# Kernel tuning notes

Hardware: AMD Instinct MI355X
Metric: run time of the kernel (lower is better)

The kernel has to match this reference:

```python
import jax, jax.numpy as jnp
import numpy as np

N_USERS = 17449
N_ITEMS = 48676
N = N_USERS + N_ITEMS  # 66125 nodes
H = 2    # heads
C = 64   # out_channels per head
D_IN = 64
E = 2_000_000
NEG_SLOPE = 0.2


def setup_inputs() -> dict:
    key = jax.random.key(0)
    ks = jax.random.split(key, 7)
    edge_index = jax.random.randint(ks[0], (2, E), 0, N, dtype=jnp.int32)
    # xavier-normal-ish init for embeddings and GAT params
    users_feature = jax.random.normal(ks[1], (N_USERS, D_IN), dtype=jnp.float32) * 0.1
    items_feature = jax.random.normal(ks[2], (N_ITEMS, D_IN), dtype=jnp.float32) * 0.1
    W = jax.random.normal(ks[3], (D_IN, H * C), dtype=jnp.float32) * (1.0 / np.sqrt(D_IN))
    att_src = jax.random.normal(ks[4], (H, C), dtype=jnp.float32) * 0.1
    att_dst = jax.random.normal(ks[5], (H, C), dtype=jnp.float32) * 0.1
    bias = jnp.zeros((H * C,), dtype=jnp.float32)
    return {
        "edge_index": edge_index,
        "users_feature": users_feature,
        "items_feature": items_feature,
        "W": W,
        "att_src": att_src,
        "att_dst": att_dst,
        "bias": bias,
    }


def reference(edge_index, users_feature, items_feature, W, att_src, att_dst, bias):
    # node features: [N, D_IN]
    x = jnp.concatenate([users_feature, items_feature], axis=0)
    # linear transform -> per-head features [N, H, C]
    h = (x @ W).reshape(N, H, C)
    # per-node attention logits [N, H]
    a_src = jnp.einsum("nhc,hc->nh", h, att_src)
    a_dst = jnp.einsum("nhc,hc->nh", h, att_dst)
    # add self loops (PyG GATConv default)
    loops = jnp.arange(N, dtype=edge_index.dtype)
    src = jnp.concatenate([edge_index[0], loops])
    dst = jnp.concatenate([edge_index[1], loops])
    # per-edge attention score [E+N, H]
    e = jax.nn.leaky_relu(a_src[src] + a_dst[dst], negative_slope=NEG_SLOPE)
    # segment softmax over destination node
    m = jax.lax.stop_gradient(jax.ops.segment_max(e, dst, num_segments=N))
    ex = jnp.exp(e - m[dst])
    denom = jax.ops.segment_sum(ex, dst, num_segments=N)
    alpha = ex / (denom[dst] + 1e-16)
    # scatter-add weighted source features -> [N, H, C]
    out = jax.ops.segment_sum(alpha[:, :, None] * h[src], dst, num_segments=N)
    # concat heads + bias -> [N, H*C]
    return out.reshape(N, H * C) + bias
```

## Files before the change

kernel.cpp:

```cpp
#include <hip/hip_runtime.h>
#include <hip/hip_fp16.h>
#include <math.h>

#define NEG_SLOPE 0.2f
#define BSHIFT 6
#define BNODES 64
#define MAXB 1056
#define CAP 2816
#define BIN_E 4096
#define SG_THREADS 256
#define RPT (CAP / SG_THREADS)

typedef unsigned short ushort8_v __attribute__((ext_vector_type(8)));
typedef short  short8_v  __attribute__((ext_vector_type(8)));
typedef float  float4_v  __attribute__((ext_vector_type(4)));

__device__ __forceinline__ unsigned short f2bf(float f) {
    unsigned u = __float_as_uint(f);
    u = (u + 0x7FFFu + ((u >> 16) & 1u)) >> 16;
    return (unsigned short)u;
}
__device__ __forceinline__ float bf2f(unsigned short b) {
    return __uint_as_float(((unsigned)b) << 16);
}
__device__ __forceinline__ float lrelu(float x) {
    return x > 0.f ? x : NEG_SLOPE * x;
}
__device__ __forceinline__ unsigned f2h_bits(float f) {
    __half_raw hr = __half_raw(__float2half_rn(f));
    return (unsigned)hr.x;
}
__device__ __forceinline__ float h2f_bits(unsigned short u) {
    __half_raw hr; hr.x = u;
    return __half2float(__half(hr));
}

__global__ __launch_bounds__(512) void k_xform_bin(
        const float* __restrict__ users,
        const float* __restrict__ items,
        const float* __restrict__ W,
        const float* __restrict__ att_src,
        const float* __restrict__ att_dst,
        unsigned short* __restrict__ hb,
        float* __restrict__ a_src,
        float* __restrict__ a_dst,
        const int* __restrict__ src,
        const int* __restrict__ dst,
        int* __restrict__ tails,
        int* __restrict__ stage_g,
        int nedges, int nbuckets, int n_users, int N,
        int nxf, int ntotal)
{
    __shared__ __align__(16) char smem[3 * MAXB * 4 + BIN_E * 4 + BIN_E * 2];

    const int tid  = threadIdx.x;
    const int lane = tid & 63;
    const int wid  = tid >> 6;

    const int bid = blockIdx.x;
    const long long num = (long long)nxf;
    const int xf_before = (int)(((long long)bid * num) / ntotal);
    const bool is_xf = ((((long long)(bid + 1) * num) / ntotal) > xf_before);

    if (!is_xf) {
        const int bin_id = bid - xf_before;
        int* cnt     = (int*)smem;
        int* runoff  = cnt + MAXB;
        int* cursor  = runoff + MAXB;
        int* stage   = cursor + MAXB;
        unsigned short* sb = (unsigned short*)(stage + BIN_E);

        const int base = bin_id * BIN_E;
        const int nvalid = min(BIN_E, nedges - base);

        for (int i = tid; i < nbuckets; i += 512) cnt[i] = 0;
        __syncthreads();

        int myrec[BIN_E / 512];
        int myb[BIN_E / 512];
        #pragma unroll
        for (int k = 0; k < BIN_E / 512; ++k) {
            int i = base + k * 512 + tid;
            if (i < nedges) {
                const int d = dst[i];
                myrec[k] = src[i] | ((d & (BNODES - 1)) << 17);
                myb[k] = d >> BSHIFT;
                atomicAdd(&cnt[myb[k]], 1);
            } else {
                myb[k] = -1;
            }
        }
        __syncthreads();

        if (wid == 0) {
            int running = 0;
            for (int b2 = 0; b2 < nbuckets; b2 += 64) {
                int idx = b2 + lane;
                int v = (idx < nbuckets) ? cnt[idx] : 0;
                int incl = v;
                #pragma unroll
                for (int off = 1; off < 64; off <<= 1) {
                    int t = __shfl_up(incl, off);
                    if (lane >= off) incl += t;
                }
                if (idx < nbuckets) runoff[idx] = running + incl - v;
                running += __shfl(incl, 63);
            }
        }
        __syncthreads();

        for (int i = tid; i < nbuckets; i += 512) cursor[i] = runoff[i];
        __syncthreads();

        #pragma unroll
        for (int k = 0; k < BIN_E / 512; ++k) {
            if (myb[k] >= 0) {
                int pos = atomicAdd(&cursor[myb[k]], 1);
                stage[pos] = myrec[k];
                sb[pos] = (unsigned short)myb[k];
            }
        }

        for (int i = tid; i < nbuckets; i += 512)
            if (cnt[i] > 0) {
                const int rb = atomicAdd(&tails[i], cnt[i]);
                runoff[i] = rb - runoff[i];
            }
        __syncthreads();

        for (int i = tid; i < nvalid; i += 512) {
            const int b = sb[i];
            const int idx = runoff[b] + i;
            if (idx < CAP)
                stage_g[(size_t)b * CAP + idx] = stage[i];
        }
        return;
    }

    unsigned short (*tile)[130] = (unsigned short (*)[130])smem;
    const int blk  = xf_before;
    const int quad = lane >> 4;
    const int l16  = lane & 15;
    const int tb   = blk * 128 + wid * 16;

    short8_v bfrag[8][2];
    #pragma unroll
    for (int t = 0; t < 8; ++t)
        #pragma unroll
        for (int h2 = 0; h2 < 2; ++h2)
            #pragma unroll
            for (int j = 0; j < 8; ++j)
                bfrag[t][h2][j] = (short)f2bf(
                    W[(h2 * 32 + quad * 8 + j) * 128 + t * 16 + l16]);

    float atts[8], attd[8];
    #pragma unroll
    for (int t = 0; t < 8; ++t) {
        atts[t] = att_src[t * 16 + l16];
        attd[t] = att_dst[t * 16 + l16];
    }

    const int arow = tb + l16;
    short8_v a0 = (short8_v)0, a1 = (short8_v)0;
    if (arow < N) {
        const float* xr = (arow < n_users)
            ? (users + (size_t)arow * 64)
            : (items + (size_t)(arow - n_users) * 64);
        const float4_v x0 = *reinterpret_cast<const float4_v*>(xr + quad * 8);
        const float4_v x1 = *reinterpret_cast<const float4_v*>(xr + quad * 8 + 4);
        const float4_v x2 = *reinterpret_cast<const float4_v*>(xr + 32 + quad * 8);
        const float4_v x3 = *reinterpret_cast<const float4_v*>(xr + 32 + quad * 8 + 4);
        #pragma unroll
        for (int j = 0; j < 4; ++j) {
            a0[j]     = (short)f2bf(x0[j]);
            a0[j + 4] = (short)f2bf(x1[j]);
            a1[j]     = (short)f2bf(x2[j]);
            a1[j + 4] = (short)f2bf(x3[j]);
        }
    }

    float4_v acc[8];
    #pragma unroll
    for (int t = 0; t < 8; ++t) {
        acc[t] = (float4_v)0.f;
        acc[t] = __builtin_amdgcn_mfma_f32_16x16x32_bf16(a0, bfrag[t][0], acc[t], 0, 0, 0);
        acc[t] = __builtin_amdgcn_mfma_f32_16x16x32_bf16(a1, bfrag[t][1], acc[t], 0, 0, 0);
    }

    const int wrow0 = tb + quad * 4;
    float s0[4] = {0,0,0,0}, s1[4] = {0,0,0,0};
    float d0[4] = {0,0,0,0}, d1[4] = {0,0,0,0};
    #pragma unroll
    for (int t = 0; t < 8; ++t) {
        #pragma unroll
        for (int r = 0; r < 4; ++r) {
            const float v = acc[t][r];
            if (t < 4) { s0[r] = fmaf(v, atts[t], s0[r]);
                         d0[r] = fmaf(v, attd[t], d0[r]); }
            else       { s1[r] = fmaf(v, atts[t], s1[r]);
                         d1[r] = fmaf(v, attd[t], d1[r]); }
            tile[wid * 16 + quad * 4 + r][t * 16 + l16] = f2bf(v);
        }
    }

    #pragma unroll
    for (int off = 1; off < 16; off <<= 1) {
        #pragma unroll
        for (int r = 0; r < 4; ++r) {
            s0[r] += __shfl_xor(s0[r], off);
            s1[r] += __shfl_xor(s1[r], off);
            d0[r] += __shfl_xor(d0[r], off);
            d1[r] += __shfl_xor(d1[r], off);
        }
    }
    if (l16 == 0) {
        #pragma unroll
        for (int r = 0; r < 4; ++r) {
            const int row = wrow0 + r;
            if (row < N) {
                a_src[row * 2]     = s0[r];
                a_src[row * 2 + 1] = s1[r];
                a_dst[row * 2]     = d0[r];
                a_dst[row * 2 + 1] = d1[r];
            }
        }
    }

    __syncthreads();
    const int base_node = blk * 128;
    const int nrem = min(128, N - base_node);
    for (int k = tid; k < nrem * 16; k += 512) {
        const int n = k >> 4, g = k & 15;
        ushort8_v v;
        #pragma unroll
        for (int j = 0; j < 8; ++j) v[j] = tile[n][g * 8 + j];
        *reinterpret_cast<ushort8_v*>(
            hb + (size_t)(base_node + n) * 128 + g * 8) = v;
    }
}

__global__ __launch_bounds__(SG_THREADS) void k_sort_gather(
        const int* __restrict__ stage_g,
        const int* __restrict__ tails,
        const float* __restrict__ a_src,
        const float* __restrict__ a_dst,
        const unsigned short* __restrict__ hb,
        const float* __restrict__ bias,
        float* __restrict__ out,
        int N)
{
    __shared__ int cnt[BNODES];
    __shared__ int off[BNODES];
    __shared__ int cursor[BNODES];
    __shared__ float adst[BNODES][2];
    __shared__ int2 lsorted[CAP];

    const int b    = blockIdx.x;
    const int tid  = threadIdx.x;
    const int lane = tid & 63;
    const int wid  = tid >> 6;
    const int node0  = b << BSHIFT;
    const int nnodes = min(BNODES, N - node0);
    const int nrec = min(tails[b], CAP);
    const int* bucket = stage_g + (size_t)b * CAP;

    if (tid < BNODES) {
        cnt[tid] = 0;
        if (tid < nnodes) {
            const float2 ad = *reinterpret_cast<const float2*>(
                a_dst + 2 * (node0 + tid));
            adst[tid][0] = ad.x;
            adst[tid][1] = ad.y;
        } else {
            adst[tid][0] = adst[tid][1] = 0.f;
        }
    }
    __syncthreads();

    int myrec[RPT];
    #pragma unroll
    for (int k = 0; k < RPT; ++k) {
        const int i = k * SG_THREADS + tid;
        if (i < nrec) {
            const int r = bucket[i];
            myrec[k] = r;
            atomicAdd(&cnt[(r >> 17) & (BNODES - 1)], 1);
        } else {
            myrec[k] = -1;
        }
    }
    __syncthreads();

    if (wid == 0) {
        const int v = cnt[lane];
        int incl = v;
        #pragma unroll
        for (int o = 1; o < 64; o <<= 1) {
            int t = __shfl_up(incl, o);
            if (lane >= o) incl += t;
        }
        off[lane] = incl - v;
        cursor[lane] = incl - v;
    }
    __syncthreads();

    #pragma unroll
    for (int k = 0; k < RPT; ++k) {
        const int r = myrec[k];
        if (r >= 0) {
            const int s = r & 0x1FFFF;
            const int n = (r >> 17) & (BNODES - 1);
            const float2 as2 = *reinterpret_cast<const float2*>(a_src + 2 * s);
            const unsigned e0 = f2h_bits(__expf(lrelu(as2.x + adst[n][0])));
            const unsigned e1 = f2h_bits(__expf(lrelu(as2.y + adst[n][1])));
            const int pos = atomicAdd(&cursor[n], 1);
            if (pos < CAP) {
                int2 rec;
                rec.x = (int)((e1 << 16) | e0);
                rec.y = s;
                lsorted[pos] = rec;
            }
        }
    }
    __syncthreads();

    const int q  = lane >> 4;
    const int sl = lane & 15;
    const int hd = sl >> 3;

    for (int n = wid; n < nnodes; n += 4) {
        const int d = node0 + n;
        const float2 as2 = *reinterpret_cast<const float2*>(a_src + 2 * d);
        const float exs0 = __expf(lrelu(as2.x + adst[n][0]));
        const float exs1 = __expf(lrelu(as2.y + adst[n][1]));
        const int start = off[n];
        const int cnt1  = cnt[n] + 1;

        float acc[8];
        #pragma unroll
        for (int i = 0; i < 8; ++i) acc[i] = 0.f;
        float den = 0.f;

        #pragma unroll 4
        for (int v = q; v < cnt1; v += 4) {
            int s; float ex;
            if (v == 0) {
                s = d;  ex = hd ? exs1 : exs0;
            } else {
                const int2 r = lsorted[start + v - 1];
                s = r.y;
                const unsigned eb = (unsigned)r.x;
                ex = h2f_bits(hd ? (unsigned short)(eb >> 16)
                                 : (unsigned short)(eb & 0xFFFFu));
            }
            const ushort8_v hv = *reinterpret_cast<const ushort8_v*>(
                hb + (size_t)s * 128 + sl * 8);
            den += ex;
            #pragma unroll
            for (int i = 0; i < 8; ++i)
                acc[i] = fmaf(ex, bf2f(hv[i]), acc[i]);
        }

        #pragma unroll
        for (int o = 16; o <= 32; o <<= 1) {
            #pragma unroll
            for (int i = 0; i < 8; ++i) acc[i] += __shfl_xor(acc[i], o);
            den += __shfl_xor(den, o);
        }

        if (q == 0) {
            const float inv = 1.f / (den + 1e-16f);
            float4 o0, o1;
            o0.x = acc[0] * inv + bias[sl * 8 + 0];
            o0.y = acc[1] * inv + bias[sl * 8 + 1];
            o0.z = acc[2] * inv + bias[sl * 8 + 2];
            o0.w = acc[3] * inv + bias[sl * 8 + 3];
            o1.x = acc[4] * inv + bias[sl * 8 + 4];
            o1.y = acc[5] * inv + bias[sl * 8 + 5];
            o1.z = acc[6] * inv + bias[sl * 8 + 6];
            o1.w = acc[7] * inv + bias[sl * 8 + 7];
            float* op = out + (size_t)d * 128 + sl * 8;
            *reinterpret_cast<float4*>(op)     = o0;
            *reinterpret_cast<float4*>(op + 4) = o1;
        }
    }
}

extern "C" void kernel_launch(void* const* d_in, const int* in_sizes, int n_in,
                              void* d_out, int out_size, void* d_ws, size_t ws_size,
                              hipStream_t stream) {
    const int*   edge  = (const int*)  d_in[0];
    const float* users = (const float*)d_in[1];
    const float* items = (const float*)d_in[2];
    const float* W     = (const float*)d_in[3];
    const float* att_s = (const float*)d_in[4];
    const float* att_d = (const float*)d_in[5];
    const float* bias  = (const float*)d_in[6];

    const int E       = in_sizes[0] / 2;
    const int n_users = in_sizes[1] / 64;
    const int n_items = in_sizes[2] / 64;
    const int N       = n_users + n_items;
    const int nbuckets = (N + BNODES - 1) >> BSHIFT;

    float* out = (float*)d_out;

    char* ws = (char*)d_ws;
    unsigned short* hb = (unsigned short*)ws;
    ws += (size_t)N * 128 * sizeof(unsigned short);
    int*   stage    = (int*)ws;    ws += (size_t)MAXB * CAP * sizeof(int);
    float* a_src    = (float*)ws;  ws += (size_t)N * 2 * sizeof(float);
    float* a_dst    = (float*)ws;  ws += (size_t)N * 2 * sizeof(float);
    int*   tails    = (int*)ws;

    const int* src = edge;
    const int* dst = edge + E;

    hipMemsetAsync(tails, 0, MAXB * sizeof(int), stream);

    const int nbin = (E + BIN_E - 1) / BIN_E;
    const int nxf  = (N + 127) / 128;
    const int ntotal = nbin + nxf;
    k_xform_bin<<<ntotal, 512, 0, stream>>>(
        users, items, W, att_s, att_d, hb, a_src, a_dst,
        src, dst, tails, stage, E, nbuckets, n_users, N, nxf, ntotal);

    k_sort_gather<<<nbuckets, SG_THREADS, 0, stream>>>(
        stage, tails, a_src, a_dst, hb, bias, out, N);
}
```

Baseline: 210.4 us.

## Split each gather bucket across two blocks by node half

Each 64-node bucket is now processed by two blocks, each handling 32 destination nodes and filtering bucket records by bit 22 of the record. This doubles the grid size and shrinks shared memory per block (LCAP 1600 instead of CAP 2816), which is meant to raise occupancy and parallelism in the gather phase. In exchange both blocks read the whole bucket from global memory. The local capacity is smaller, so a heavy half could overflow and drop records.

```diff
diff --git a/kernel.cpp b/kernel.cpp
--- a/kernel.cpp
+++ b/kernel.cpp
@@ -10,6 +10,8 @@
 #define BIN_E 4096
 #define SG_THREADS 256
 #define RPT (CAP / SG_THREADS)
+#define HNODES 32
+#define LCAP 1600
 
 typedef unsigned short ushort8_v __attribute__((ext_vector_type(8)));
 typedef short  short8_v  __attribute__((ext_vector_type(8)));
@@ -249,22 +251,24 @@
         float* __restrict__ out,
         int N)
 {
-    __shared__ int cnt[BNODES];
-    __shared__ int off[BNODES];
-    __shared__ int cursor[BNODES];
-    __shared__ float adst[BNODES][2];
-    __shared__ int2 lsorted[CAP];
-
-    const int b    = blockIdx.x;
+    __shared__ int cnt[HNODES];
+    __shared__ int off[HNODES];
+    __shared__ int cursor[HNODES];
+    __shared__ float adst[HNODES][2];
+    __shared__ int2 lsorted[LCAP];
+
+    const int blk  = blockIdx.x;
+    const int b    = blk >> 1;
+    const int half = blk & 1;
     const int tid  = threadIdx.x;
     const int lane = tid & 63;
     const int wid  = tid >> 6;
-    const int node0  = b << BSHIFT;
-    const int nnodes = min(BNODES, N - node0);
+    const int node0  = (b << BSHIFT) + half * HNODES;
+    const int nnodes = min(HNODES, N - node0);
     const int nrec = min(tails[b], CAP);
     const int* bucket = stage_g + (size_t)b * CAP;
 
-    if (tid < BNODES) {
+    if (tid < HNODES) {
         cnt[tid] = 0;
         if (tid < nnodes) {
             const float2 ad = *reinterpret_cast<const float2*>(
@@ -281,21 +285,23 @@
     #pragma unroll
     for (int k = 0; k < RPT; ++k) {
         const int i = k * SG_THREADS + tid;
+        int keep = -1;
         if (i < nrec) {
             const int r = bucket[i];
-            myrec[k] = r;
-            atomicAdd(&cnt[(r >> 17) & (BNODES - 1)], 1);
-        } else {
-            myrec[k] = -1;
-        }
+            if (((r >> 22) & 1) == half) {
+                keep = r;
+                atomicAdd(&cnt[(r >> 17) & (HNODES - 1)], 1);
+            }
+        }
+        myrec[k] = keep;
     }
     __syncthreads();
 
-    if (wid == 0) {
+    if (wid == 0 && lane < HNODES) {
         const int v = cnt[lane];
         int incl = v;
         #pragma unroll
-        for (int o = 1; o < 64; o <<= 1) {
+        for (int o = 1; o < HNODES; o <<= 1) {
             int t = __shfl_up(incl, o);
             if (lane >= o) incl += t;
         }
@@ -309,12 +315,12 @@
         const int r = myrec[k];
         if (r >= 0) {
             const int s = r & 0x1FFFF;
-            const int n = (r >> 17) & (BNODES - 1);
+            const int n = (r >> 17) & (HNODES - 1);
             const float2 as2 = *reinterpret_cast<const float2*>(a_src + 2 * s);
             const unsigned e0 = f2h_bits(__expf(lrelu(as2.x + adst[n][0])));
             const unsigned e1 = f2h_bits(__expf(lrelu(as2.y + adst[n][1])));
             const int pos = atomicAdd(&cursor[n], 1);
-            if (pos < CAP) {
+            if (pos < LCAP) {
                 int2 rec;
                 rec.x = (int)((e1 << 16) | e0);
                 rec.y = s;
@@ -425,6 +431,6 @@
         users, items, W, att_s, att_d, hb, a_src, a_dst,
         src, dst, tails, stage, E, nbuckets, n_users, N, nxf, ntotal);
 
-    k_sort_gather<<<nbuckets, SG_THREADS, 0, stream>>>(
+    k_sort_gather<<<2 * nbuckets, SG_THREADS, 0, stream>>>(
         stage, tails, a_src, a_dst, hb, bias, out, N);
 }
```

After: 224.5 us. 1.07x slower.

## Fuse memset, bin/transform and sort-gather into one persistent cooperative kernel

Applied to the files above, without the earlier changes.

Replaces the memset and two kernel launches with a single cooperative persistent kernel. It zeroes the counters in-kernel, pulls bin and transform work items from an atomic queue, does a grid-wide sync, then pulls sort-gather buckets from a second queue. Block size drops from 512 to 256 threads and transform tiles shrink to 64 rows. The aim is to remove launch gaps and the tail imbalance between stages, at the cost of grid-sync overhead and a capped persistent grid size.

```diff
diff --git a/kernel.cpp b/kernel.cpp
--- a/kernel.cpp
+++ b/kernel.cpp
@@ -1,4 +1,5 @@
 #include <hip/hip_runtime.h>
+#include <hip/hip_cooperative_groups.h>
 #include <hip/hip_fp16.h>
 #include <math.h>
 
@@ -8,8 +9,10 @@
 #define MAXB 1056
 #define CAP 2816
 #define BIN_E 4096
-#define SG_THREADS 256
-#define RPT (CAP / SG_THREADS)
+#define THREADS 256
+#define RPT_SG (CAP / THREADS)
+#define RPT_BIN (BIN_E / THREADS)
+#define SMEM_BYTES 37248
 
 typedef unsigned short ushort8_v __attribute__((ext_vector_type(8)));
 typedef short  short8_v  __attribute__((ext_vector_type(8)));
@@ -35,113 +38,100 @@
     return __half2float(__half(hr));
 }
 
-__global__ __launch_bounds__(512) void k_xform_bin(
-        const float* __restrict__ users,
-        const float* __restrict__ items,
-        const float* __restrict__ W,
-        const float* __restrict__ att_src,
-        const float* __restrict__ att_dst,
-        unsigned short* __restrict__ hb,
-        float* __restrict__ a_src,
-        float* __restrict__ a_dst,
-        const int* __restrict__ src,
-        const int* __restrict__ dst,
-        int* __restrict__ tails,
-        int* __restrict__ stage_g,
-        int nedges, int nbuckets, int n_users, int N,
-        int nxf, int ntotal)
-{
-    __shared__ __align__(16) char smem[3 * MAXB * 4 + BIN_E * 4 + BIN_E * 2];
+struct FusedArgs {
+    const float* users; const float* items; const float* W;
+    const float* att_src; const float* att_dst;
+    unsigned short* hb; float* a_src; float* a_dst;
+    const int* src; const int* dst;
+    int* tails; int* stage_g; int* ctrs;
+    const float* bias; float* out;
+    int E, n_users, N, nbin, nxf, nbuckets;
+};
+
+__device__ void bin_part(char* smem, const FusedArgs& a, int bin_id) {
+    int* cnt     = (int*)smem;
+    int* runoff  = cnt + MAXB;
+    int* cursor  = runoff + MAXB;
+    int* stage   = cursor + MAXB;
+    unsigned short* sb = (unsigned short*)(stage + BIN_E);
 
     const int tid  = threadIdx.x;
     const int lane = tid & 63;
     const int wid  = tid >> 6;
-
-    const int bid = blockIdx.x;
-    const long long num = (long long)nxf;
-    const int xf_before = (int)(((long long)bid * num) / ntotal);
-    const bool is_xf = ((((long long)(bid + 1) * num) / ntotal) > xf_before);
-
-    if (!is_xf) {
-        const int bin_id = bid - xf_before;
-        int* cnt     = (int*)smem;
-        int* runoff  = cnt + MAXB;
-        int* cursor  = runoff + MAXB;
-        int* stage   = cursor + MAXB;
-        unsigned short* sb = (unsigned short*)(stage + BIN_E);
-
-        const int base = bin_id * BIN_E;
-        const int nvalid = min(BIN_E, nedges - base);
-
-        for (int i = tid; i < nbuckets; i += 512) cnt[i] = 0;
-        __syncthreads();
-
-        int myrec[BIN_E / 512];
-        int myb[BIN_E / 512];
-        #pragma unroll
-        for (int k = 0; k < BIN_E / 512; ++k) {
-            int i = base + k * 512 + tid;
-            if (i < nedges) {
-                const int d = dst[i];
-                myrec[k] = src[i] | ((d & (BNODES - 1)) << 17);
-                myb[k] = d >> BSHIFT;
-                atomicAdd(&cnt[myb[k]], 1);
-            } else {
-                myb[k] = -1;
+    const int base = bin_id * BIN_E;
+    const int nvalid = min(BIN_E, a.E - base);
+
+    for (int i = tid; i < a.nbuckets; i += THREADS) cnt[i] = 0;
+    __syncthreads();
+
+    int myrec[RPT_BIN];
+    int myb[RPT_BIN];
+    #pragma unroll
+    for (int k = 0; k < RPT_BIN; ++k) {
+        int i = base + k * THREADS + tid;
+        if (i < a.E) {
+            const int d = a.dst[i];
+            myrec[k] = a.src[i] | ((d & (BNODES - 1)) << 17);
+            myb[k] = d >> BSHIFT;
+            atomicAdd(&cnt[myb[k]], 1);
+        } else {
+            myb[k] = -1;
+        }
+    }
+    __syncthreads();
+
+    if (wid == 0) {
+        int running = 0;
+        for (int b2 = 0; b2 < a.nbuckets; b2 += 64) {
+            int idx = b2 + lane;
+            int v = (idx < a.nbuckets) ? cnt[idx] : 0;
+            int incl = v;
+            #pragma unroll
+            for (int off = 1; off < 64; off <<= 1) {
+                int t = __shfl_up(incl, off);
+                if (lane >= off) incl += t;
             }
-        }
-        __syncthreads();
-
-        if (wid == 0) {
-            int running = 0;
-            for (int b2 = 0; b2 < nbuckets; b2 += 64) {
-                int idx = b2 + lane;
-                int v = (idx < nbuckets) ? cnt[idx] : 0;
-                int incl = v;
-                #pragma unroll
-                for (int off = 1; off < 64; off <<= 1) {
-                    int t = __shfl_up(incl, off);
-                    if (lane >= off) incl += t;
-                }
-                if (idx < nbuckets) runoff[idx] = running + incl - v;
-                running += __shfl(incl, 63);
-            }
-        }
-        __syncthreads();
-
-        for (int i = tid; i < nbuckets; i += 512) cursor[i] = runoff[i];
-        __syncthreads();
-
-        #pragma unroll
-        for (int k = 0; k < BIN_E / 512; ++k) {
-            if (myb[k] >= 0) {
-                int pos = atomicAdd(&cursor[myb[k]], 1);
-                stage[pos] = myrec[k];
-                sb[pos] = (unsigned short)myb[k];
-            }
-        }
-
-        for (int i = tid; i < nbuckets; i += 512)
-            if (cnt[i] > 0) {
-                const int rb = atomicAdd(&tails[i], cnt[i]);
-                runoff[i] = rb - runoff[i];
-            }
-        __syncthreads();
-
-        for (int i = tid; i < nvalid; i += 512) {
-            const int b = sb[i];
-            const int idx = runoff[b] + i;
-            if (idx < CAP)
-                stage_g[(size_t)b * CAP + idx] = stage[i];
-        }
-        return;
-    }
-
+            if (idx < a.nbuckets) runoff[idx] = running + incl - v;
+            running += __shfl(incl, 63);
+        }
+    }
+    __syncthreads();
+
+    for (int i = tid; i < a.nbuckets; i += THREADS) cursor[i] = runoff[i];
+    __syncthreads();
+
+    #pragma unroll
+    for (int k = 0; k < RPT_BIN; ++k) {
+        if (myb[k] >= 0) {
+            int pos = atomicAdd(&cursor[myb[k]], 1);
+            stage[pos] = myrec[k];
+            sb[pos] = (unsigned short)myb[k];
+        }
+    }
+
+    for (int i = tid; i < a.nbuckets; i += THREADS)
+        if (cnt[i] > 0) {
+            const int rb = atomicAdd(&a.tails[i], cnt[i]);
+            runoff[i] = rb - runoff[i];
+        }
+    __syncthreads();
+
+    for (int i = tid; i < nvalid; i += THREADS) {
+        const int b = sb[i];
+        const int idx = runoff[b] + i;
+        if (idx < CAP)
+            a.stage_g[(size_t)b * CAP + idx] = stage[i];
+    }
+}
+
+__device__ void xform_part(char* smem, const FusedArgs& a, int blk) {
     unsigned short (*tile)[130] = (unsigned short (*)[130])smem;
-    const int blk  = xf_before;
+    const int tid  = threadIdx.x;
+    const int lane = tid & 63;
+    const int wid  = tid >> 6;
     const int quad = lane >> 4;
     const int l16  = lane & 15;
-    const int tb   = blk * 128 + wid * 16;
+    const int tb   = blk * 64 + wid * 16;
 
     short8_v bfrag[8][2];
     #pragma unroll
@@ -151,21 +141,21 @@
             #pragma unroll
             for (int j = 0; j < 8; ++j)
                 bfrag[t][h2][j] = (short)f2bf(
-                    W[(h2 * 32 + quad * 8 + j) * 128 + t * 16 + l16]);
+                    a.W[(h2 * 32 + quad * 8 + j) * 128 + t * 16 + l16]);
 
     float atts[8], attd[8];
     #pragma unroll
     for (int t = 0; t < 8; ++t) {
-        atts[t] = att_src[t * 16 + l16];
-        attd[t] = att_dst[t * 16 + l16];
+        atts[t] = a.att_src[t * 16 + l16];
+        attd[t] = a.att_dst[t * 16 + l16];
     }
 
     const int arow = tb + l16;
     short8_v a0 = (short8_v)0, a1 = (short8_v)0;
-    if (arow < N) {
-        const float* xr = (arow < n_users)
-            ? (users + (size_t)arow * 64)
-            : (items + (size_t)(arow - n_users) * 64);
+    if (arow < a.N) {
+        const float* xr = (arow < a.n_users)
+            ? (a.users + (size_t)arow * 64)
+            : (a.items + (size_t)(arow - a.n_users) * 64);
         const float4_v x0 = *reinterpret_cast<const float4_v*>(xr + quad * 8);
         const float4_v x1 = *reinterpret_cast<const float4_v*>(xr + quad * 8 + 4);
         const float4_v x2 = *reinterpret_cast<const float4_v*>(xr + 32 + quad * 8);
@@ -217,58 +207,47 @@
         #pragma unroll
         for (int r = 0; r < 4; ++r) {
             const int row = wrow0 + r;
-            if (row < N) {
-                a_src[row * 2]     = s0[r];
-                a_src[row * 2 + 1] = s1[r];
-                a_dst[row * 2]     = d0[r];
-                a_dst[row * 2 + 1] = d1[r];
+            if (row < a.N) {
+                a.a_src[row * 2]     = s0[r];
+                a.a_src[row * 2 + 1] = s1[r];
+                a.a_dst[row * 2]     = d0[r];
+                a.a_dst[row * 2 + 1] = d1[r];
             }
         }
     }
 
     __syncthreads();
-    const int base_node = blk * 128;
-    const int nrem = min(128, N - base_node);
-    for (int k = tid; k < nrem * 16; k += 512) {
+    const int nrem = min(64, a.N - blk * 64);
+    for (int k = tid; k < nrem * 16; k += THREADS) {
         const int n = k >> 4, g = k & 15;
         ushort8_v v;
         #pragma unroll
         for (int j = 0; j < 8; ++j) v[j] = tile[n][g * 8 + j];
         *reinterpret_cast<ushort8_v*>(
-            hb + (size_t)(base_node + n) * 128 + g * 8) = v;
-    }
-}
-
-__global__ __launch_bounds__(SG_THREADS) void k_sort_gather(
-        const int* __restrict__ stage_g,
-        const int* __restrict__ tails,
-        const float* __restrict__ a_src,
-        const float* __restrict__ a_dst,
-        const unsigned short* __restrict__ hb,
-        const float* __restrict__ bias,
-        float* __restrict__ out,
-        int N)
-{
-    __shared__ int cnt[BNODES];
-    __shared__ int off[BNODES];
-    __shared__ int cursor[BNODES];
-    __shared__ float adst[BNODES][2];
-    __shared__ int2 lsorted[CAP];
-
-    const int b    = blockIdx.x;
+            a.hb + (size_t)(blk * 64 + n) * 128 + g * 8) = v;
+    }
+}
+
+__device__ void sg_part(char* smem, const FusedArgs& a, int b) {
+    int* cnt    = (int*)smem;
+    int* off    = cnt + BNODES;
+    int* cursor = off + BNODES;
+    float (*adst)[2] = (float (*)[2])(cursor + BNODES);
+    int2* lsorted = (int2*)(adst + BNODES);
+
     const int tid  = threadIdx.x;
     const int lane = tid & 63;
     const int wid  = tid >> 6;
     const int node0  = b << BSHIFT;
-    const int nnodes = min(BNODES, N - node0);
-    const int nrec = min(tails[b], CAP);
-    const int* bucket = stage_g + (size_t)b * CAP;
+    const int nnodes = min(BNODES, a.N - node0);
+    const int nrec = min(a.tails[b], CAP);
+    const int* bucket = a.stage_g + (size_t)b * CAP;
 
     if (tid < BNODES) {
         cnt[tid] = 0;
         if (tid < nnodes) {
             const float2 ad = *reinterpret_cast<const float2*>(
-                a_dst + 2 * (node0 + tid));
+                a.a_dst + 2 * (node0 + tid));
             adst[tid][0] = ad.x;
             adst[tid][1] = ad.y;
         } else {
@@ -277,10 +256,10 @@
     }
     __syncthreads();
 
-    int myrec[RPT];
-    #pragma unroll
-    for (int k = 0; k < RPT; ++k) {
-        const int i = k * SG_THREADS + tid;
+    int myrec[RPT_SG];
+    #pragma unroll
+    for (int k = 0; k < RPT_SG; ++k) {
+        const int i = k * THREADS + tid;
         if (i < nrec) {
             const int r = bucket[i];
             myrec[k] = r;
@@ -305,12 +284,12 @@
     __syncthreads();
 
     #pragma unroll
-    for (int k = 0; k < RPT; ++k) {
+    for (int k = 0; k < RPT_SG; ++k) {
         const int r = myrec[k];
         if (r >= 0) {
             const int s = r & 0x1FFFF;
             const int n = (r >> 17) & (BNODES - 1);
-            const float2 as2 = *reinterpret_cast<const float2*>(a_src + 2 * s);
+            const float2 as2 = *reinterpret_cast<const float2*>(a.a_src + 2 * s);
             const unsigned e0 = f2h_bits(__expf(lrelu(as2.x + adst[n][0])));
             const unsigned e1 = f2h_bits(__expf(lrelu(as2.y + adst[n][1])));
             const int pos = atomicAdd(&cursor[n], 1);
@@ -330,7 +309,7 @@
 
     for (int n = wid; n < nnodes; n += 4) {
         const int d = node0 + n;
-        const float2 as2 = *reinterpret_cast<const float2*>(a_src + 2 * d);
+        const float2 as2 = *reinterpret_cast<const float2*>(a.a_src + 2 * d);
         const float exs0 = __expf(lrelu(as2.x + adst[n][0]));
         const float exs1 = __expf(lrelu(as2.y + adst[n][1]));
         const int start = off[n];
@@ -354,7 +333,7 @@
                                  : (unsigned short)(eb & 0xFFFFu));
             }
             const ushort8_v hv = *reinterpret_cast<const ushort8_v*>(
-                hb + (size_t)s * 128 + sl * 8);
+                a.hb + (size_t)s * 128 + sl * 8);
             den += ex;
             #pragma unroll
             for (int i = 0; i < 8; ++i)
@@ -371,19 +350,65 @@
         if (q == 0) {
             const float inv = 1.f / (den + 1e-16f);
             float4 o0, o1;
-            o0.x = acc[0] * inv + bias[sl * 8 + 0];
-            o0.y = acc[1] * inv + bias[sl * 8 + 1];
-            o0.z = acc[2] * inv + bias[sl * 8 + 2];
-            o0.w = acc[3] * inv + bias[sl * 8 + 3];
-            o1.x = acc[4] * inv + bias[sl * 8 + 4];
-            o1.y = acc[5] * inv + bias[sl * 8 + 5];
-            o1.z = acc[6] * inv + bias[sl * 8 + 6];
-            o1.w = acc[7] * inv + bias[sl * 8 + 7];
-            float* op = out + (size_t)d * 128 + sl * 8;
+            o0.x = acc[0] * inv + a.bias[sl * 8 + 0];
+            o0.y = acc[1] * inv + a.bias[sl * 8 + 1];
+            o0.z = acc[2] * inv + a.bias[sl * 8 + 2];
+            o0.w = acc[3] * inv + a.bias[sl * 8 + 3];
+            o1.x = acc[4] * inv + a.bias[sl * 8 + 4];
+            o1.y = acc[5] * inv + a.bias[sl * 8 + 5];
+            o1.z = acc[6] * inv + a.bias[sl * 8 + 6];
+            o1.w = acc[7] * inv + a.bias[sl * 8 + 7];
+            float* op = a.out + (size_t)d * 128 + sl * 8;
             *reinterpret_cast<float4*>(op)     = o0;
             *reinterpret_cast<float4*>(op + 4) = o1;
         }
     }
+}
+
+__global__ __launch_bounds__(THREADS) void k_fused(FusedArgs a) {
+    __shared__ __align__(16) char smem[SMEM_BYTES];
+    __shared__ int s_item;
+
+    const int tid = threadIdx.x;
+
+    for (int i = blockIdx.x * THREADS + tid; i < MAXB + 2;
+         i += gridDim.x * THREADS) {
+        if (i < MAXB) a.tails[i] = 0;
+        else         a.ctrs[i - MAXB] = 0;
+    }
+    cooperative_groups::this_grid().sync();
+
+    const int nitems = a.nbin + a.nxf;
+    for (;;) {
+        __syncthreads();
+        if (tid == 0) s_item = atomicAdd(&a.ctrs[0], 1);
+        __syncthreads();
+        const int item = s_item;
+        if (item >= nitems) break;
+        if (item < a.nbin) bin_part(smem, a, item);
+        else               xform_part(smem, a, item - a.nbin);
+    }
+    cooperative_groups::this_grid().sync();
+
+    for (;;) {
+        __syncthreads();
+        if (tid == 0) s_item = atomicAdd(&a.ctrs[1], 1);
+        __syncthreads();
+        const int b = s_item;
+        if (b >= a.nbuckets) break;
+        sg_part(smem, a, b);
+    }
+}
+
+__global__ __launch_bounds__(THREADS) void k_xb_fb(FusedArgs a) {
+    __shared__ __align__(16) char smem[SMEM_BYTES];
+    const int item = blockIdx.x;
+    if (item < a.nbin) bin_part(smem, a, item);
+    else               xform_part(smem, a, item - a.nbin);
+}
+__global__ __launch_bounds__(THREADS) void k_sg_fb(FusedArgs a) {
+    __shared__ __align__(16) char smem[SMEM_BYTES];
+    sg_part(smem, a, blockIdx.x);
 }
 
 extern "C" void kernel_launch(void* const* d_in, const int* in_sizes, int n_in,
@@ -411,20 +436,47 @@
     int*   stage    = (int*)ws;    ws += (size_t)MAXB * CAP * sizeof(int);
     float* a_src    = (float*)ws;  ws += (size_t)N * 2 * sizeof(float);
     float* a_dst    = (float*)ws;  ws += (size_t)N * 2 * sizeof(float);
-    int*   tails    = (int*)ws;
-
-    const int* src = edge;
-    const int* dst = edge + E;
-
-    hipMemsetAsync(tails, 0, MAXB * sizeof(int), stream);
-
-    const int nbin = (E + BIN_E - 1) / BIN_E;
-    const int nxf  = (N + 127) / 128;
-    const int ntotal = nbin + nxf;
-    k_xform_bin<<<ntotal, 512, 0, stream>>>(
-        users, items, W, att_s, att_d, hb, a_src, a_dst,
-        src, dst, tails, stage, E, nbuckets, n_users, N, nxf, ntotal);
-
-    k_sort_gather<<<nbuckets, SG_THREADS, 0, stream>>>(
-        stage, tails, a_src, a_dst, hb, bias, out, N);
-}
+    int*   tails    = (int*)ws;    ws += MAXB * sizeof(int);
+    int*   ctrs     = (int*)ws;
+
+    FusedArgs fa;
+    fa.users = users; fa.items = items; fa.W = W;
+    fa.att_src = att_s; fa.att_dst = att_d;
+    fa.hb = hb; fa.a_src = a_src; fa.a_dst = a_dst;
+    fa.src = edge; fa.dst = edge + E;
+    fa.tails = tails; fa.stage_g = stage; fa.ctrs = ctrs;
+    fa.bias = bias; fa.out = out;
+    fa.E = E; fa.n_users = n_users; fa.N = N;
+    fa.nbin = (E + BIN_E - 1) / BIN_E;
+    fa.nxf  = (N + 63) / 64;
+    fa.nbuckets = nbuckets;
+
+    static int s_grid = -1;
+    if (s_grid < 0) {
+        int dev = 0;
+        hipGetDevice(&dev);
+        hipDeviceProp_t prop;
+        int per_cu = 0;
+        if (hipGetDeviceProperties(&prop, dev) == hipSuccess &&
+            hipOccupancyMaxActiveBlocksPerMultiprocessor(
+                &per_cu, k_fused, THREADS, 0) == hipSuccess && per_cu > 0) {
+            s_grid = per_cu * prop.multiProcessorCount;
+            if (s_grid > 1536) s_grid = 1536;
+        } else {
+            s_grid = 0;
+        }
+    }
+
+    bool launched = false;
+    if (s_grid > 0) {
+        void* kargs[] = { (void*)&fa };
+        hipError_t err = hipLaunchCooperativeKernel(
+            k_fused, dim3(s_grid), dim3(THREADS), kargs, 0, stream);
+        launched = (err == hipSuccess);
+    }
+    if (!launched) {
+        hipMemsetAsync(tails, 0, (MAXB + 2) * sizeof(int), stream);
+        k_xb_fb<<<fa.nbin + fa.nxf, THREADS, 0, stream>>>(fa);
+        k_sg_fb<<<nbuckets, THREADS, 0, stream>>>(fa);
+    }
+}
```

New measurement: 249.9 us. 1.19x slower.
